# Optimization experiments

Hardware: AMD Instinct MI355X
Metric: run time of the kernel (lower is better)

## Reference

```python
import jax, jax.numpy as jnp
import numpy as np

V = 50000
E = 800000
HIDDEN = 128
NUM_BASES = 64
D_MIN, D_MAX = 0.0, 25.0  # squared-distance range for radius=5.0


def setup_inputs() -> dict:
    key = jax.random.key(0)
    ks = jax.random.split(key, 10)
    s = 1.0 / np.sqrt(HIDDEN)
    sb = 1.0 / np.sqrt(NUM_BASES)
    return {
        "X": jax.random.normal(ks[0], (V, HIDDEN), jnp.float32),
        "R": jax.random.normal(ks[1], (V, 3), jnp.float32),
        "src": jax.random.randint(ks[2], (E,), 0, V),
        "dest": jax.random.randint(ks[3], (E,), 0, V),
        # filter-generating MLP (no bias, per nn.Linear(..., bias=False))
        "W1": jax.random.uniform(ks[4], (NUM_BASES, HIDDEN), jnp.float32, -sb, sb),
        "W2": jax.random.uniform(ks[5], (HIDDEN, HIDDEN), jnp.float32, -s, s),
        # update MLP (with bias)
        "U1": jax.random.uniform(ks[6], (HIDDEN, HIDDEN), jnp.float32, -s, s),
        "b1": jax.random.uniform(ks[7], (HIDDEN,), jnp.float32, -s, s),
        "U2": jax.random.uniform(ks[8], (HIDDEN, HIDDEN), jnp.float32, -s, s),
        "b2": jax.random.uniform(ks[9], (HIDDEN,), jnp.float32, -s, s),
    }


def _rbf(d):
    # Gaussian RBF expansion: centers linspaced over [D_MIN, D_MAX]
    centers = jnp.linspace(D_MIN, D_MAX, NUM_BASES, dtype=d.dtype)
    width = (D_MAX - D_MIN) / (NUM_BASES - 1)
    return jnp.exp(-((d[:, None] - centers) ** 2) / (2.0 * width * width))  # [E, num_bases]


def reference(X, R, src, dest, W1, W2, U1, b1, U2, b2):
    # squared pairwise distance per edge (original: .square().sum(-1), no sqrt)
    D_ij = jnp.sum((R[src] - R[dest]) ** 2, axis=-1)  # [E]
    # filter-generating network: RBF -> Linear -> ReLU -> Linear -> ReLU
    M = jax.nn.relu(_rbf(D_ij) @ W1)
    M = jax.nn.relu(M @ W2)  # [E, d_h]
    # gather-multiply-scatter: continuous-filter convolution
    H = jax.ops.segment_sum(X[src] * M, dest, num_segments=X.shape[0])  # [V, d_h]
    # update MLP (note: self.W(X) in the original is dead code, overwritten)
    out = jax.nn.relu(H @ U1 + b1) @ U2 + b2
    return out
```

## Files before the change

### kernel.cpp

```cpp
#include <hip/hip_runtime.h>
#include <hip/hip_bf16.h>
#include <hip/hip_fp16.h>

#define HIDDEN 128
#define NB 64
#define TG 8192
#define TPTS (TG + 1)
#define TMAX 32.0f
#define TINV ((float)TG / TMAX)
#define CAP 64
#define NB1 1024
#define BINCAP 20

typedef _Float16 f16;
typedef _Float16 f16x8 __attribute__((ext_vector_type(8)));
typedef float floatx4 __attribute__((ext_vector_type(4)));
typedef unsigned short ushort;
typedef unsigned int uint;

__global__ __launch_bounds__(256) void megaprep(
    const int* __restrict__ src, const int* __restrict__ dest,
    const float* __restrict__ R, float4* __restrict__ Rp,
    const float* __restrict__ X, f16* __restrict__ Xh,
    const float* __restrict__ W1, const float* __restrict__ W2,
    f16* __restrict__ Th,
    const float* __restrict__ U1, const float* __restrict__ U2,
    f16* __restrict__ U1p, f16* __restrict__ U2p,
    uint* __restrict__ staging, uint* __restrict__ cnt1,
    int E, int V, int XB, int TB, int RB, int EPB) {
    __shared__ uint smem[256 + 256 * BINCAP];
    const int b = blockIdx.x;
    const int tid = threadIdx.x;
    if (b < NB1) {
        uint* scur = smem;
        uint* sbin = smem + 256;
        scur[tid] = 0;
        __syncthreads();
        const int e0 = b * EPB;
        const int e1 = min(e0 + EPB, E);
        for (int e = e0 + tid; e < e1; e += 256) {
            const uint s = (uint)src[e];
            const uint d = (uint)dest[e];
            const uint bin = d >> 8;
            const uint k = atomicAdd(&scur[bin], 1u);
            if (k < BINCAP) sbin[bin * BINCAP + k] = s | ((d & 255u) << 16);
        }
        __syncthreads();
        const uint n = min(scur[tid], (uint)BINCAP);
        uint4* dst = (uint4*)(staging + ((size_t)b * 256 + tid) * BINCAP);
        const uint4* sp = (const uint4*)(sbin + tid * BINCAP);
        for (uint k4 = 0; k4 * 4 < n; ++k4) dst[k4] = sp[k4];
        cnt1[b * 256 + tid] = n;
    } else if (b < NB1 + XB) {
        const int idx = ((b - NB1) * 256 + tid) * 8;
        if (idx < V * HIDDEN) {
            const float4 v0 = *(const float4*)(X + idx);
            const float4 v1 = *(const float4*)(X + idx + 4);
            f16x8 h;
            h[0] = (f16)v0.x; h[1] = (f16)v0.y; h[2] = (f16)v0.z; h[3] = (f16)v0.w;
            h[4] = (f16)v1.x; h[5] = (f16)v1.y; h[6] = (f16)v1.z; h[7] = (f16)v1.w;
            *(f16x8*)(Xh + idx) = h;
        }
    } else if (b < NB1 + XB + TB) {
        f16* h2 = (f16*)smem;
        const int lane = tid & 63;
        const int w = tid >> 6;
        const int rt = w & 1;
        const int ct0 = (w >> 1) * 4;
        const int lrow = lane & 15;
        const int lk = lane >> 4;
        const int g0 = (b - NB1 - XB) * 32;
        const float d2a = (float)(g0 + rt * 16 + lrow) * (TMAX / (float)TG);
        const float wid = 25.0f / 63.0f;
        f16x8 a[4];
#pragma unroll
        for (int kt = 0; kt < 2; ++kt)
#pragma unroll
            for (int j = 0; j < 8; ++j) {
                const float z = d2a - wid * (float)(kt * 32 + lk * 8 + j);
                a[kt][j] = (f16)expf(-(z * z) / (2.0f * wid * wid));
            }
        floatx4 acc[4];
#pragma unroll
        for (int c = 0; c < 4; ++c) acc[c] = (floatx4){0.f, 0.f, 0.f, 0.f};
#pragma unroll
        for (int c = 0; c < 4; ++c) {
            const int col = (ct0 + c) * 16 + lrow;
#pragma unroll
            for (int kt = 0; kt < 2; ++kt) {
                f16x8 bf;
#pragma unroll
                for (int j = 0; j < 8; ++j)
                    bf[j] = (f16)W1[(kt * 32 + lk * 8 + j) * HIDDEN + col];
                acc[c] = __builtin_amdgcn_mfma_f32_16x16x32_f16(a[kt], bf, acc[c], 0, 0, 0);
            }
        }
#pragma unroll
        for (int c = 0; c < 4; ++c) {
            const int col = (ct0 + c) * 16 + lrow;
#pragma unroll
            for (int rr = 0; rr < 4; ++rr)
                h2[(rt * 16 + lk * 4 + rr) * 136 + col] = (f16)fmaxf(acc[c][rr], 0.0f);
        }
        __syncthreads();
        f16x8 a2[4];
#pragma unroll
        for (int kt = 0; kt < 4; ++kt)
            a2[kt] = *(const f16x8*)&h2[(rt * 16 + lrow) * 136 + kt * 32 + lk * 8];
#pragma unroll
        for (int c = 0; c < 4; ++c) acc[c] = (floatx4){0.f, 0.f, 0.f, 0.f};
#pragma unroll
        for (int c = 0; c < 4; ++c) {
            const int col = (ct0 + c) * 16 + lrow;
#pragma unroll
            for (int kt = 0; kt < 4; ++kt) {
                f16x8 bf;
#pragma unroll
                for (int j = 0; j < 8; ++j)
                    bf[j] = (f16)W2[(kt * 32 + lk * 8 + j) * HIDDEN + col];
                acc[c] = __builtin_amdgcn_mfma_f32_16x16x32_f16(a2[kt], bf, acc[c], 0, 0, 0);
            }
        }
#pragma unroll
        for (int c = 0; c < 4; ++c) {
            const int col = (ct0 + c) * 16 + lrow;
#pragma unroll
            for (int rr = 0; rr < 4; ++rr) {
                const int g = g0 + rt * 16 + lk * 4 + rr;
                if (g <= TG) Th[(size_t)g * 128 + col] = (f16)fmaxf(acc[c][rr], 0.0f);
            }
        }
    } else if (b < NB1 + XB + TB + RB) {
        const int v = (b - NB1 - XB - TB) * 256 + tid;
        if (v < V) Rp[v] = make_float4(R[3 * v], R[3 * v + 1], R[3 * v + 2], 0.f);
    } else {
        const int ub = b - NB1 - XB - TB - RB;
        const int i = (ub & 63) * 256 + tid;
        const int j = i & 7;
        const int l = (i >> 3) & 63;
        const int ktct = i >> 9;
        const int kt = ktct >> 3, ct = ktct & 7;
        const int srcidx = (kt * 32 + (l >> 4) * 8 + j) * HIDDEN + ct * 16 + (l & 15);
        if (ub < 64) U1p[i] = (f16)U1[srcidx];
        else         U2p[i] = (f16)U2[srcidx];
    }
}

__global__ __launch_bounds__(256) void bucketize(
    const uint* __restrict__ staging, const uint* __restrict__ cnt1,
    ushort* __restrict__ eps, int* __restrict__ deg, int V) {
    __shared__ ushort bucket[256 * CAP];
    __shared__ uint lcur[256];
    const int r = blockIdx.x;
    const int tid = threadIdx.x;
    lcur[tid] = 0;
    __syncthreads();
    for (int b = tid; b < NB1; b += 256) {
        uint n = cnt1[b * 256 + r];
        n = min(n, (uint)BINCAP);
        const uint* seg = staging + ((size_t)b * 256 + r) * BINCAP;
        for (uint k = 0; k < n; ++k) {
            const uint e = seg[k];
            const uint dl = e >> 16;
            const uint kk = atomicAdd(&lcur[dl], 1u);
            if (kk < CAP) bucket[dl * CAP + kk] = (ushort)(e & 0xFFFFu);
        }
    }
    __syncthreads();
    const uint4* bs = (const uint4*)bucket;
    uint4* ed = (uint4*)(eps + (size_t)r * (256 * CAP));
    for (int i = tid; i < 256 * CAP / 8; i += 256) ed[i] = bs[i];
    const int d = r * 256 + tid;
    if (d < V) deg[d] = (int)min(lcur[tid], (uint)CAP);
}

__global__ __launch_bounds__(256) void gather_accum(
    const int* __restrict__ deg, const ushort* __restrict__ eps,
    const float4* __restrict__ Rp,
    const f16* __restrict__ Xh, const f16* __restrict__ Th,
    f16* __restrict__ Hf, int V) {
    const int node = blockIdx.x * 4 + (threadIdx.x >> 6);
    const int lane = threadIdx.x & 63;
    if (node >= V) return;
    const int cl = lane & 15;
    const int es = lane >> 4;
    const int dn = deg[node];
    const float4 rn = Rp[node];
    float acc[8];
#pragma unroll
    for (int i = 0; i < 8; ++i) acc[i] = 0.0f;
    const char* thb = (const char*)Th + cl * 16;
    const char* xhb = (const char*)Xh + cl * 16;
    const size_t base = (size_t)node << 6;
    for (int off = 0; off < dn; off += 64) {
        const int n = min(64, dn - off);
        int my_s = 0;
        if (lane < n) my_s = (int)eps[base + off + lane];
        const float4 rs = Rp[my_s];
        const float dx = rs.x - rn.x;
        const float dy = rs.y - rn.y;
        const float dz = rs.z - rn.z;
        const float D2 = fmaf(dx, dx, fmaf(dy, dy, dz * dz));
        const int my_g = (lane < n) ? min((int)fmaf(D2, TINV, 0.5f), TG) : TG;
        const int nst2 = ((n + 3) >> 2) + 1 & ~1;
        for (int j = 0; j < nst2; j += 2) {
            const int idx0 = 4 * j + es;
            const int idx1 = idx0 + 4;
            const int s0 = __shfl(my_s, idx0);
            const int g0 = __shfl(my_g, idx0);
            const int s1 = __shfl(my_s, idx1);
            const int g1 = __shfl(my_g, idx1);
            const f16x8 m0 = *(const f16x8*)(thb + g0 * 256);
            const f16x8 x0 = *(const f16x8*)(xhb + s0 * 256);
            const f16x8 m1 = *(const f16x8*)(thb + g1 * 256);
            const f16x8 x1 = *(const f16x8*)(xhb + s1 * 256);
#pragma unroll
            for (int i = 0; i < 8; ++i)
                acc[i] = fmaf((float)m0[i], (float)x0[i], acc[i]);
#pragma unroll
            for (int i = 0; i < 8; ++i)
                acc[i] = fmaf((float)m1[i], (float)x1[i], acc[i]);
        }
    }
#pragma unroll
    for (int i = 0; i < 8; ++i) {
        acc[i] += __shfl_xor(acc[i], 16);
        acc[i] += __shfl_xor(acc[i], 32);
    }
    if (es == 0) {
        f16x8 h;
#pragma unroll
        for (int i = 0; i < 8; ++i) h[i] = (f16)acc[i];
        *(f16x8*)((char*)Hf + node * 256 + cl * 16) = h;
    }
}

__global__ __launch_bounds__(256) void node_mlp(
    const f16x8* __restrict__ Hf8, const f16x8* __restrict__ U1p,
    const float* __restrict__ b1, const f16x8* __restrict__ U2p,
    const float* __restrict__ b2, float* __restrict__ out, int V) {
    __shared__ f16 h2[32][136];
    const int tid = threadIdx.x;
    const int lane = tid & 63;
    const int w = tid >> 6;
    const int rt = w & 1;
    const int ct0 = (w >> 1) * 4;
    const int r0 = blockIdx.x * 32;
    const int lrow = lane & 15;
    const int lk = lane >> 4;

    const int arow = min(r0 + rt * 16 + lrow, V - 1);
    f16x8 a[4];
#pragma unroll
    for (int kt = 0; kt < 4; ++kt)
        a[kt] = Hf8[(size_t)arow * 16 + kt * 4 + lk];

    floatx4 acc[4];
#pragma unroll
    for (int c = 0; c < 4; ++c) acc[c] = (floatx4){0.f, 0.f, 0.f, 0.f};
#pragma unroll
    for (int c = 0; c < 4; ++c) {
        const int ct = ct0 + c;
#pragma unroll
        for (int kt = 0; kt < 4; ++kt) {
            const f16x8 bf = U1p[(kt * 8 + ct) * 64 + lane];
            acc[c] = __builtin_amdgcn_mfma_f32_16x16x32_f16(a[kt], bf, acc[c], 0, 0, 0);
        }
    }
#pragma unroll
    for (int c = 0; c < 4; ++c) {
        const int col = (ct0 + c) * 16 + lrow;
        const float bb = b1[col];
#pragma unroll
        for (int rr = 0; rr < 4; ++rr) {
            const int row = rt * 16 + lk * 4 + rr;
            h2[row][col] = (f16)fmaxf(acc[c][rr] + bb, 0.0f);
        }
    }
    __syncthreads();

#pragma unroll
    for (int kt = 0; kt < 4; ++kt)
        a[kt] = *(const f16x8*)&h2[rt * 16 + lrow][kt * 32 + lk * 8];
#pragma unroll
    for (int c = 0; c < 4; ++c) acc[c] = (floatx4){0.f, 0.f, 0.f, 0.f};
#pragma unroll
    for (int c = 0; c < 4; ++c) {
        const int ct = ct0 + c;
#pragma unroll
        for (int kt = 0; kt < 4; ++kt) {
            const f16x8 bf = U2p[(kt * 8 + ct) * 64 + lane];
            acc[c] = __builtin_amdgcn_mfma_f32_16x16x32_f16(a[kt], bf, acc[c], 0, 0, 0);
        }
    }
#pragma unroll
    for (int c = 0; c < 4; ++c) {
        const int col = (ct0 + c) * 16 + lrow;
        const float bb = b2[col];
#pragma unroll
        for (int rr = 0; rr < 4; ++rr) {
            const int row = r0 + rt * 16 + lk * 4 + rr;
            if (row < V) out[(size_t)row * HIDDEN + col] = acc[c][rr] + bb;
        }
    }
}

extern "C" void kernel_launch(void* const* d_in, const int* in_sizes, int n_in,
                              void* d_out, int out_size, void* d_ws, size_t ws_size,
                              hipStream_t stream) {
    const float* X = (const float*)d_in[0];
    const float* R = (const float*)d_in[1];
    const int* src = (const int*)d_in[2];
    const int* dest = (const int*)d_in[3];
    const float* W1 = (const float*)d_in[4];
    const float* W2 = (const float*)d_in[5];
    const float* U1 = (const float*)d_in[6];
    const float* b1 = (const float*)d_in[7];
    const float* U2 = (const float*)d_in[8];
    const float* b2 = (const float*)d_in[9];

    const int V = in_sizes[0] / HIDDEN;
    const int E = in_sizes[2];
    const int XB = (V * HIDDEN / 8 + 255) / 256;
    const int TB = (TPTS + 31) / 32;
    const int RB = (V + 255) / 256;
    const int NR = (V + 255) >> 8;
    const int EPB = (E + NB1 - 1) / NB1;

    char* base = (char*)d_ws;
    f16* Hf = (f16*)base;                       base += (size_t)V * HIDDEN * sizeof(f16);
    f16* Th = (f16*)base;                       base += ((size_t)TPTS * 128 * sizeof(f16) + 255) & ~255;
    f16* Xh = (f16*)base;                       base += (size_t)V * HIDDEN * sizeof(f16);
    ushort* eps = (ushort*)base;                base += (size_t)NR * 256 * CAP * sizeof(ushort);
    float4* Rp = (float4*)base;                 base += (size_t)V * sizeof(float4);
    f16* U1p = (f16*)base;                      base += (size_t)HIDDEN * HIDDEN * sizeof(f16);
    f16* U2p = (f16*)base;                      base += (size_t)HIDDEN * HIDDEN * sizeof(f16);
    uint* staging = (uint*)base;                base += (size_t)NB1 * 256 * BINCAP * sizeof(uint);
    uint* cnt1 = (uint*)base;                   base += (size_t)NB1 * 256 * sizeof(uint);
    int* deg = (int*)base;                      base += (size_t)NR * 256 * sizeof(int);

    megaprep<<<NB1 + XB + TB + RB + 128, 256, 0, stream>>>(
        src, dest, R, Rp, X, Xh, W1, W2, Th, U1, U2, U1p, U2p,
        staging, cnt1, E, V, XB, TB, RB, EPB);
    bucketize<<<NR, 256, 0, stream>>>(staging, cnt1, eps, deg, V);
    gather_accum<<<(V + 3) / 4, 256, 0, stream>>>(deg, eps, (const float4*)Rp,
                                                  Xh, Th, Hf, V);
    node_mlp<<<(V + 31) / 32, 256, 0, stream>>>((const f16x8*)Hf, (const f16x8*)U1p,
                                                b1, (const f16x8*)U2p, b2,
                                                (float*)d_out, V);
}
```

Measured before the change: 95.56 us.

## Fuse edge gather-accumulate with node update MLP in one kernel

Merges the gather/accumulate kernel and the node MLP kernel into one kernel. Each 512-thread block aggregates 32 nodes into shared memory and then runs both MFMA layers on them, so the fp16 H intermediate no longer goes through global memory and one launch is dropped. The per-node loop now assumes degree is at most 64 (CAP), which drops the outer chunk loop. In exchange the block is larger, uses more shared memory, and the MLP phase waits on the slowest node's gather in each block.

After: 95.99 us. No clear change (+0.5%).

```diff
diff --git a/kernel.cpp b/kernel.cpp
--- a/kernel.cpp
+++ b/kernel.cpp
@@ -174,35 +174,42 @@
     if (d < V) deg[d] = (int)min(lcur[tid], (uint)CAP);
 }
 
-__global__ __launch_bounds__(256) void gather_accum(
+__global__ __launch_bounds__(512) void gather_mlp(
     const int* __restrict__ deg, const ushort* __restrict__ eps,
     const float4* __restrict__ Rp,
     const f16* __restrict__ Xh, const f16* __restrict__ Th,
-    f16* __restrict__ Hf, int V) {
-    const int node = blockIdx.x * 4 + (threadIdx.x >> 6);
-    const int lane = threadIdx.x & 63;
-    if (node >= V) return;
+    const f16x8* __restrict__ U1p, const float* __restrict__ b1,
+    const f16x8* __restrict__ U2p, const float* __restrict__ b2,
+    float* __restrict__ out, int V) {
+    __shared__ f16 hg[32 * 136];
+    __shared__ f16 h2[32 * 136];
+    const int tid = threadIdx.x;
+    const int lane = tid & 63;
+    const int wid = tid >> 6;
+    const int nb = blockIdx.x * 32;
+
     const int cl = lane & 15;
     const int es = lane >> 4;
-    const int dn = deg[node];
-    const float4 rn = Rp[node];
-    float acc[8];
-#pragma unroll
-    for (int i = 0; i < 8; ++i) acc[i] = 0.0f;
     const char* thb = (const char*)Th + cl * 16;
     const char* xhb = (const char*)Xh + cl * 16;
-    const size_t base = (size_t)node << 6;
-    for (int off = 0; off < dn; off += 64) {
-        const int n = min(64, dn - off);
+#pragma unroll
+    for (int q = 0; q < 4; ++q) {
+        const int lrowi = wid * 4 + q;
+        const int node = nb + lrowi;
+        const int dn = (node < V) ? deg[node] : 0;
+        const float4 rn = Rp[min(node, V - 1)];
+        float acc[8];
+#pragma unroll
+        for (int i = 0; i < 8; ++i) acc[i] = 0.0f;
         int my_s = 0;
-        if (lane < n) my_s = (int)eps[base + off + lane];
+        if (lane < dn) my_s = (int)eps[((size_t)node << 6) + lane];
         const float4 rs = Rp[my_s];
         const float dx = rs.x - rn.x;
         const float dy = rs.y - rn.y;
         const float dz = rs.z - rn.z;
         const float D2 = fmaf(dx, dx, fmaf(dy, dy, dz * dz));
-        const int my_g = (lane < n) ? min((int)fmaf(D2, TINV, 0.5f), TG) : TG;
-        const int nst2 = ((n + 3) >> 2) + 1 & ~1;
+        const int my_g = (lane < dn) ? min((int)fmaf(D2, TINV, 0.5f), TG) : TG;
+        const int nst2 = (((dn + 3) >> 2) + 1) & ~1;
         for (int j = 0; j < nst2; j += 2) {
             const int idx0 = 4 * j + es;
             const int idx1 = idx0 + 4;
@@ -221,86 +228,75 @@
             for (int i = 0; i < 8; ++i)
                 acc[i] = fmaf((float)m1[i], (float)x1[i], acc[i]);
         }
-    }
-#pragma unroll
-    for (int i = 0; i < 8; ++i) {
-        acc[i] += __shfl_xor(acc[i], 16);
-        acc[i] += __shfl_xor(acc[i], 32);
-    }
-    if (es == 0) {
-        f16x8 h;
-#pragma unroll
-        for (int i = 0; i < 8; ++i) h[i] = (f16)acc[i];
-        *(f16x8*)((char*)Hf + node * 256 + cl * 16) = h;
-    }
-}
-
-__global__ __launch_bounds__(256) void node_mlp(
-    const f16x8* __restrict__ Hf8, const f16x8* __restrict__ U1p,
-    const float* __restrict__ b1, const f16x8* __restrict__ U2p,
-    const float* __restrict__ b2, float* __restrict__ out, int V) {
-    __shared__ f16 h2[32][136];
-    const int tid = threadIdx.x;
-    const int lane = tid & 63;
-    const int w = tid >> 6;
-    const int rt = w & 1;
-    const int ct0 = (w >> 1) * 4;
-    const int r0 = blockIdx.x * 32;
+#pragma unroll
+        for (int i = 0; i < 8; ++i) {
+            acc[i] += __shfl_xor(acc[i], 16);
+            acc[i] += __shfl_xor(acc[i], 32);
+        }
+        if (es == 0) {
+            f16x8 h;
+#pragma unroll
+            for (int i = 0; i < 8; ++i) h[i] = (f16)acc[i];
+            *(f16x8*)&hg[lrowi * 136 + cl * 8] = h;
+        }
+    }
+    __syncthreads();
+
+    const int rt = wid & 1;
+    const int ctp = wid >> 1;
     const int lrow = lane & 15;
     const int lk = lane >> 4;
 
-    const int arow = min(r0 + rt * 16 + lrow, V - 1);
     f16x8 a[4];
 #pragma unroll
     for (int kt = 0; kt < 4; ++kt)
-        a[kt] = Hf8[(size_t)arow * 16 + kt * 4 + lk];
-
-    floatx4 acc[4];
-#pragma unroll
-    for (int c = 0; c < 4; ++c) acc[c] = (floatx4){0.f, 0.f, 0.f, 0.f};
-#pragma unroll
-    for (int c = 0; c < 4; ++c) {
-        const int ct = ct0 + c;
+        a[kt] = *(const f16x8*)&hg[(rt * 16 + lrow) * 136 + kt * 32 + lk * 8];
+    floatx4 acc2[2];
+#pragma unroll
+    for (int c = 0; c < 2; ++c) acc2[c] = (floatx4){0.f, 0.f, 0.f, 0.f};
+#pragma unroll
+    for (int c = 0; c < 2; ++c) {
+        const int ct = ctp * 2 + c;
 #pragma unroll
         for (int kt = 0; kt < 4; ++kt) {
             const f16x8 bf = U1p[(kt * 8 + ct) * 64 + lane];
-            acc[c] = __builtin_amdgcn_mfma_f32_16x16x32_f16(a[kt], bf, acc[c], 0, 0, 0);
-        }
-    }
-#pragma unroll
-    for (int c = 0; c < 4; ++c) {
-        const int col = (ct0 + c) * 16 + lrow;
+            acc2[c] = __builtin_amdgcn_mfma_f32_16x16x32_f16(a[kt], bf, acc2[c], 0, 0, 0);
+        }
+    }
+#pragma unroll
+    for (int c = 0; c < 2; ++c) {
+        const int col = (ctp * 2 + c) * 16 + lrow;
         const float bb = b1[col];
 #pragma unroll
         for (int rr = 0; rr < 4; ++rr) {
             const int row = rt * 16 + lk * 4 + rr;
-            h2[row][col] = (f16)fmaxf(acc[c][rr] + bb, 0.0f);
+            h2[row * 136 + col] = (f16)fmaxf(acc2[c][rr] + bb, 0.0f);
         }
     }
     __syncthreads();
 
 #pragma unroll
     for (int kt = 0; kt < 4; ++kt)
-        a[kt] = *(const f16x8*)&h2[rt * 16 + lrow][kt * 32 + lk * 8];
-#pragma unroll
-    for (int c = 0; c < 4; ++c) acc[c] = (floatx4){0.f, 0.f, 0.f, 0.f};
-#pragma unroll
-    for (int c = 0; c < 4; ++c) {
-        const int ct = ct0 + c;
+        a[kt] = *(const f16x8*)&h2[(rt * 16 + lrow) * 136 + kt * 32 + lk * 8];
+#pragma unroll
+    for (int c = 0; c < 2; ++c) acc2[c] = (floatx4){0.f, 0.f, 0.f, 0.f};
+#pragma unroll
+    for (int c = 0; c < 2; ++c) {
+        const int ct = ctp * 2 + c;
 #pragma unroll
         for (int kt = 0; kt < 4; ++kt) {
             const f16x8 bf = U2p[(kt * 8 + ct) * 64 + lane];
-            acc[c] = __builtin_amdgcn_mfma_f32_16x16x32_f16(a[kt], bf, acc[c], 0, 0, 0);
-        }
-    }
-#pragma unroll
-    for (int c = 0; c < 4; ++c) {
-        const int col = (ct0 + c) * 16 + lrow;
+            acc2[c] = __builtin_amdgcn_mfma_f32_16x16x32_f16(a[kt], bf, acc2[c], 0, 0, 0);
+        }
+    }
+#pragma unroll
+    for (int c = 0; c < 2; ++c) {
+        const int col = (ctp * 2 + c) * 16 + lrow;
         const float bb = b2[col];
 #pragma unroll
         for (int rr = 0; rr < 4; ++rr) {
-            const int row = r0 + rt * 16 + lk * 4 + rr;
-            if (row < V) out[(size_t)row * HIDDEN + col] = acc[c][rr] + bb;
+            const int row = nb + rt * 16 + lk * 4 + rr;
+            if (row < V) out[(size_t)row * HIDDEN + col] = acc2[c][rr] + bb;
         }
     }
 }
@@ -328,7 +324,6 @@
     const int EPB = (E + NB1 - 1) / NB1;
 
     char* base = (char*)d_ws;
-    f16* Hf = (f16*)base;                       base += (size_t)V * HIDDEN * sizeof(f16);
     f16* Th = (f16*)base;                       base += ((size_t)TPTS * 128 * sizeof(f16) + 255) & ~255;
     f16* Xh = (f16*)base;                       base += (size_t)V * HIDDEN * sizeof(f16);
     ushort* eps = (ushort*)base;                base += (size_t)NR * 256 * CAP * sizeof(ushort);
@@ -343,9 +338,8 @@
         src, dest, R, Rp, X, Xh, W1, W2, Th, U1, U2, U1p, U2p,
         staging, cnt1, E, V, XB, TB, RB, EPB);
     bucketize<<<NR, 256, 0, stream>>>(staging, cnt1, eps, deg, V);
-    gather_accum<<<(V + 3) / 4, 256, 0, stream>>>(deg, eps, (const float4*)Rp,
-                                                  Xh, Th, Hf, V);
-    node_mlp<<<(V + 31) / 32, 256, 0, stream>>>((const f16x8*)Hf, (const f16x8*)U1p,
-                                                b1, (const f16x8*)U2p, b2,
-                                                (float*)d_out, V);
+    gather_mlp<<<(V + 31) / 32, 512, 0, stream>>>(deg, eps, (const float4*)Rp,
+                                                  Xh, Th, (const f16x8*)U1p, b1,
+                                                  (const f16x8*)U2p, b2,
+                                                  (float*)d_out, V);
 }
```
